# Kernel tuning notes

Measured on AMD Instinct MI355X. Metric: run time of the kernel, lower is better.

The kernel has to match this reference:

```python
import jax, jax.numpy as jnp
import numpy as np

EPS = 1e-8  # torch F.cosine_similarity eps


def setup_inputs() -> dict:
    key = jax.random.key(0)
    k1, k2 = jax.random.split(key)
    z = jax.random.normal(k1, (32768, 2048), dtype=jnp.float32)
    expert_keys = jax.random.normal(k2, (64, 2048), dtype=jnp.float32)
    return {"z": z, "expert_keys": expert_keys}


def reference(z, expert_keys):
    # cosine similarity: (z . ek) / max(||z||*||ek||, eps)  -> [N, E]
    dots = jnp.einsum("nd,ed->ne", z, expert_keys)
    z_norm = jnp.linalg.norm(z, axis=-1)            # [N]
    e_norm = jnp.linalg.norm(expert_keys, axis=-1)  # [E]
    similarity = dots / jnp.maximum(z_norm[:, None] * e_norm[None, :], EPS)
    # softmax over experts, then weighted combination of expert keys -> [N, D]
    weighted_expert = jax.nn.softmax(similarity, axis=-1) @ expert_keys
    return similarity, weighted_expert
```

## Files before the change

### kernel.cpp

```cpp
#include <hip/hip_runtime.h>
#include <hip/hip_bf16.h>

typedef __attribute__((ext_vector_type(4))) float f32x4;
typedef __attribute__((ext_vector_type(8))) short bf16x8;

#define NROWS 32768
#define DIM   2048
#define NEXP  64

__device__ __forceinline__ short f2bf(float f) {
    __hip_bfloat16 h = __float2bfloat16(f);
    short s;
    __builtin_memcpy(&s, &h, 2);
    return s;
}

__global__ __launch_bounds__(256) void prep_experts(
    const float* __restrict__ ek,
    short* __restrict__ ekbf,
    short* __restrict__ ekT,
    float* __restrict__ enorm)
{
    const int e = blockIdx.x;
    const int t = threadIdx.x;
    const float* row = ek + e * DIM;
    float ss = 0.f;
#pragma unroll
    for (int i = 0; i < 2; ++i) {
        const int c4 = t + i * 256;
        const float4 v = ((const float4*)row)[c4];
        ss += v.x * v.x + v.y * v.y + v.z * v.z + v.w * v.w;
        short4 b;
        b.x = f2bf(v.x); b.y = f2bf(v.y); b.z = f2bf(v.z); b.w = f2bf(v.w);
        *(short4*)(ekbf + e * DIM + c4 * 4) = b;
        const int d = c4 * 4;
        ekT[(d + 0) * NEXP + e] = b.x;
        ekT[(d + 1) * NEXP + e] = b.y;
        ekT[(d + 2) * NEXP + e] = b.z;
        ekT[(d + 3) * NEXP + e] = b.w;
    }
#pragma unroll
    for (int s = 1; s < 64; s <<= 1) ss += __shfl_xor(ss, s);
    __shared__ float red[4];
    if ((t & 63) == 0) red[t >> 6] = ss;
    __syncthreads();
    if (t == 0) enorm[e] = sqrtf(red[0] + red[1] + red[2] + red[3]);
}

__global__ __launch_bounds__(256) void cosmoe_main(
    const float* __restrict__ z,
    const short* __restrict__ ekbf,
    const short* __restrict__ ekT,
    const float* __restrict__ enorm,
    float* __restrict__ out_sim,
    float* __restrict__ out_wei)
{
    const int tid = threadIdx.x;
    const int w   = tid >> 6;
    const int l   = tid & 63;
    const int lr  = l & 15;
    const int lg  = l >> 4;
    const int base_row = blockIdx.x * 64;

    const float* zrow = z + (size_t)(base_row + w * 16 + lr) * DIM + lg * 8;
    f32x4 acc[4];
#pragma unroll
    for (int nt = 0; nt < 4; ++nt) acc[nt] = f32x4{0.f, 0.f, 0.f, 0.f};
    float ssq = 0.f;

    for (int kk = 0; kk < DIM / 32; ++kk) {
        const float4 a0 = *(const float4*)(zrow + kk * 32);
        const float4 a1 = *(const float4*)(zrow + kk * 32 + 4);
        ssq += a0.x * a0.x + a0.y * a0.y + a0.z * a0.z + a0.w * a0.w
             + a1.x * a1.x + a1.y * a1.y + a1.z * a1.z + a1.w * a1.w;
        bf16x8 af;
        af[0] = f2bf(a0.x); af[1] = f2bf(a0.y); af[2] = f2bf(a0.z); af[3] = f2bf(a0.w);
        af[4] = f2bf(a1.x); af[5] = f2bf(a1.y); af[6] = f2bf(a1.z); af[7] = f2bf(a1.w);
        const int koff = kk * 32 + lg * 8;
#pragma unroll
        for (int nt = 0; nt < 4; ++nt) {
            const bf16x8 bf = *(const bf16x8*)(ekbf + (nt * 16 + lr) * DIM + koff);
            acc[nt] = __builtin_amdgcn_mfma_f32_16x16x32_bf16(af, bf, acc[nt], 0, 0, 0);
        }
    }
    ssq += __shfl_xor(ssq, 16);
    ssq += __shfl_xor(ssq, 32);
    const float zn_mine = sqrtf(ssq);

    float zn_j[4];
#pragma unroll
    for (int j = 0; j < 4; ++j) zn_j[j] = __shfl(zn_mine, lg * 4 + j);
    float en_nt[4];
#pragma unroll
    for (int nt = 0; nt < 4; ++nt) en_nt[nt] = enorm[nt * 16 + lr];

    float sim[4][4];
#pragma unroll
    for (int j = 0; j < 4; ++j)
#pragma unroll
        for (int nt = 0; nt < 4; ++nt)
            sim[nt][j] = acc[nt][j] / fmaxf(zn_j[j] * en_nt[nt], 1e-8f);

#pragma unroll
    for (int j = 0; j < 4; ++j) {
        const size_t ro = (size_t)(base_row + w * 16 + lg * 4 + j) * NEXP + lr;
#pragma unroll
        for (int nt = 0; nt < 4; ++nt) out_sim[ro + nt * 16] = sim[nt][j];
    }

    float wgt[4][4];
#pragma unroll
    for (int j = 0; j < 4; ++j) {
        float mx = fmaxf(fmaxf(sim[0][j], sim[1][j]), fmaxf(sim[2][j], sim[3][j]));
#pragma unroll
        for (int s = 1; s < 16; s <<= 1) mx = fmaxf(mx, __shfl_xor(mx, s));
        float sum = 0.f;
#pragma unroll
        for (int nt = 0; nt < 4; ++nt) { wgt[nt][j] = __expf(sim[nt][j] - mx); sum += wgt[nt][j]; }
#pragma unroll
        for (int s = 1; s < 16; s <<= 1) sum += __shfl_xor(sum, s);
        const float inv = 1.0f / sum;
#pragma unroll
        for (int nt = 0; nt < 4; ++nt) wgt[nt][j] *= inv;
    }

    __shared__ __align__(16) short Wl[4][16][72];
#pragma unroll
    for (int j = 0; j < 4; ++j)
#pragma unroll
        for (int nt = 0; nt < 4; ++nt)
            Wl[w][lg * 4 + j][nt * 16 + lr] = f2bf(wgt[nt][j]);
    __syncthreads();

    bf16x8 afr[4][2];
#pragma unroll
    for (int mt = 0; mt < 4; ++mt)
#pragma unroll
        for (int ks = 0; ks < 2; ++ks)
            afr[mt][ks] = *(const bf16x8*)&Wl[mt][lr][ks * 32 + lg * 8];

    for (int ntl = 0; ntl < 32; ++ntl) {
        const int d0 = w * 512 + ntl * 16;
        const short* bp = ekT + (size_t)(d0 + lr) * NEXP + lg * 8;
        const bf16x8 b0 = *(const bf16x8*)bp;
        const bf16x8 b1 = *(const bf16x8*)(bp + 32);
        f32x4 oacc[4];
#pragma unroll
        for (int mt = 0; mt < 4; ++mt) {
            oacc[mt] = f32x4{0.f, 0.f, 0.f, 0.f};
            oacc[mt] = __builtin_amdgcn_mfma_f32_16x16x32_bf16(afr[mt][0], b0, oacc[mt], 0, 0, 0);
            oacc[mt] = __builtin_amdgcn_mfma_f32_16x16x32_bf16(afr[mt][1], b1, oacc[mt], 0, 0, 0);
        }
#pragma unroll
        for (int mt = 0; mt < 4; ++mt)
#pragma unroll
            for (int j = 0; j < 4; ++j)
                out_wei[(size_t)(base_row + mt * 16 + lg * 4 + j) * DIM + d0 + lr] = oacc[mt][j];
    }
}

extern "C" void kernel_launch(void* const* d_in, const int* in_sizes, int n_in,
                              void* d_out, int out_size, void* d_ws, size_t ws_size,
                              hipStream_t stream) {
    const float* z  = (const float*)d_in[0];
    const float* ek = (const float*)d_in[1];
    float* out_sim = (float*)d_out;
    float* out_wei = out_sim + (size_t)NROWS * NEXP;

    short* ekbf  = (short*)d_ws;
    short* ekT   = ekbf + NEXP * DIM;
    float* enorm = (float*)(ekT + DIM * NEXP);

    prep_experts<<<NEXP, 256, 0, stream>>>(ek, ekbf, ekT, enorm);
    cosmoe_main<<<NROWS / 64, 256, 0, stream>>>(z, ekbf, ekT, enorm, out_sim, out_wei);
}
```

Before: 162.2 us.

## Split fused kernel into split-K similarity and tiled softmax-combine kernels

Replaces the single fused kernel with two kernels. The first computes similarities with the K dimension split across the four waves of a block and reduced through shared memory, giving more blocks and shorter dependency chains. The second re-reads the similarity matrix, computes softmax, and multiplies by the expert keys over a 2D grid, staging outputs in LDS so each global store writes float4s across contiguous columns. In exchange the similarity output makes an extra round trip through global memory and there is one more launch.

Result: slower. 171.3 us (+5.6%).

```diff
diff --git a/kernel.cpp b/kernel.cpp
--- a/kernel.cpp
+++ b/kernel.cpp
@@ -47,12 +47,87 @@
     if (t == 0) enorm[e] = sqrtf(red[0] + red[1] + red[2] + red[3]);
 }
 
-__global__ __launch_bounds__(256) void cosmoe_main(
+__global__ __launch_bounds__(256) void sim_kernel(
     const float* __restrict__ z,
     const short* __restrict__ ekbf,
+    const float* __restrict__ enorm,
+    float* __restrict__ out_sim)
+{
+    const int tid = threadIdx.x;
+    const int w   = tid >> 6;
+    const int l   = tid & 63;
+    const int lr  = l & 15;
+    const int lg  = l >> 4;
+    const int base = blockIdx.x * 16;
+
+    __shared__ float racc[4][64][20];
+    __shared__ float rssq[4][16];
+
+    const float* zp = z    + (size_t)(base + lr) * DIM + w * 512 + lg * 8;
+    const short* ep = ekbf + (size_t)lr * DIM          + w * 512 + lg * 8;
+
+    f32x4 acc[4];
+#pragma unroll
+    for (int nt = 0; nt < 4; ++nt) acc[nt] = f32x4{0.f, 0.f, 0.f, 0.f};
+    float s0 = 0.f, s1 = 0.f;
+
+#pragma unroll 4
+    for (int c = 0; c < 16; ++c) {
+        const float4 a0 = *(const float4*)(zp + c * 32);
+        const float4 a1 = *(const float4*)(zp + c * 32 + 4);
+        s0 = fmaf(a0.x, a0.x, s0); s1 = fmaf(a0.y, a0.y, s1);
+        s0 = fmaf(a0.z, a0.z, s0); s1 = fmaf(a0.w, a0.w, s1);
+        s0 = fmaf(a1.x, a1.x, s0); s1 = fmaf(a1.y, a1.y, s1);
+        s0 = fmaf(a1.z, a1.z, s0); s1 = fmaf(a1.w, a1.w, s1);
+        bf16x8 af;
+        af[0] = f2bf(a0.x); af[1] = f2bf(a0.y); af[2] = f2bf(a0.z); af[3] = f2bf(a0.w);
+        af[4] = f2bf(a1.x); af[5] = f2bf(a1.y); af[6] = f2bf(a1.z); af[7] = f2bf(a1.w);
+#pragma unroll
+        for (int nt = 0; nt < 4; ++nt) {
+            const bf16x8 bf = *(const bf16x8*)(ep + nt * 16 * DIM + c * 32);
+            acc[nt] = __builtin_amdgcn_mfma_f32_16x16x32_bf16(af, bf, acc[nt], 0, 0, 0);
+        }
+    }
+    float ssq = s0 + s1;
+    ssq += __shfl_xor(ssq, 16);
+    ssq += __shfl_xor(ssq, 32);
+
+#pragma unroll
+    for (int nt = 0; nt < 4; ++nt)
+        *(f32x4*)&racc[w][l][nt * 4] = acc[nt];
+    if (l < 16) rssq[w][l] = ssq;
+    __syncthreads();
+
+    if (w == 0) {
+        f32x4 tot[4];
+#pragma unroll
+        for (int nt = 0; nt < 4; ++nt) {
+            tot[nt] = *(const f32x4*)&racc[0][l][nt * 4];
+#pragma unroll
+            for (int w2 = 1; w2 < 4; ++w2)
+                tot[nt] += *(const f32x4*)&racc[w2][l][nt * 4];
+        }
+        const float sq = rssq[0][lr] + rssq[1][lr] + rssq[2][lr] + rssq[3][lr];
+        const float zn = sqrtf(sq);
+        float zn_j[4];
+#pragma unroll
+        for (int j = 0; j < 4; ++j) zn_j[j] = __shfl(zn, lg * 4 + j);
+        float en_nt[4];
+#pragma unroll
+        for (int nt = 0; nt < 4; ++nt) en_nt[nt] = enorm[nt * 16 + lr];
+#pragma unroll
+        for (int j = 0; j < 4; ++j) {
+            const size_t ro = (size_t)(base + lg * 4 + j) * NEXP + lr;
+#pragma unroll
+            for (int nt = 0; nt < 4; ++nt)
+                out_sim[ro + nt * 16] = tot[nt][j] / fmaxf(zn_j[j] * en_nt[nt], 1e-8f);
+        }
+    }
+}
+
+__global__ __launch_bounds__(256) void moe_kernel(
+    const float* __restrict__ sim,
     const short* __restrict__ ekT,
-    const float* __restrict__ enorm,
-    float* __restrict__ out_sim,
     float* __restrict__ out_wei)
 {
     const int tid = threadIdx.x;
@@ -60,102 +135,80 @@
     const int l   = tid & 63;
     const int lr  = l & 15;
     const int lg  = l >> 4;
-    const int base_row = blockIdx.x * 64;
-
-    const float* zrow = z + (size_t)(base_row + w * 16 + lr) * DIM + lg * 8;
-    f32x4 acc[4];
-#pragma unroll
-    for (int nt = 0; nt < 4; ++nt) acc[nt] = f32x4{0.f, 0.f, 0.f, 0.f};
-    float ssq = 0.f;
-
-    for (int kk = 0; kk < DIM / 32; ++kk) {
-        const float4 a0 = *(const float4*)(zrow + kk * 32);
-        const float4 a1 = *(const float4*)(zrow + kk * 32 + 4);
-        ssq += a0.x * a0.x + a0.y * a0.y + a0.z * a0.z + a0.w * a0.w
-             + a1.x * a1.x + a1.y * a1.y + a1.z * a1.z + a1.w * a1.w;
-        bf16x8 af;
-        af[0] = f2bf(a0.x); af[1] = f2bf(a0.y); af[2] = f2bf(a0.z); af[3] = f2bf(a0.w);
-        af[4] = f2bf(a1.x); af[5] = f2bf(a1.y); af[6] = f2bf(a1.z); af[7] = f2bf(a1.w);
-        const int koff = kk * 32 + lg * 8;
-#pragma unroll
-        for (int nt = 0; nt < 4; ++nt) {
-            const bf16x8 bf = *(const bf16x8*)(ekbf + (nt * 16 + lr) * DIM + koff);
-            acc[nt] = __builtin_amdgcn_mfma_f32_16x16x32_bf16(af, bf, acc[nt], 0, 0, 0);
-        }
-    }
-    ssq += __shfl_xor(ssq, 16);
-    ssq += __shfl_xor(ssq, 32);
-    const float zn_mine = sqrtf(ssq);
-
-    float zn_j[4];
-#pragma unroll
-    for (int j = 0; j < 4; ++j) zn_j[j] = __shfl(zn_mine, lg * 4 + j);
-    float en_nt[4];
-#pragma unroll
-    for (int nt = 0; nt < 4; ++nt) en_nt[nt] = enorm[nt * 16 + lr];
-
-    float sim[4][4];
-#pragma unroll
-    for (int j = 0; j < 4; ++j)
-#pragma unroll
-        for (int nt = 0; nt < 4; ++nt)
-            sim[nt][j] = acc[nt][j] / fmaxf(zn_j[j] * en_nt[nt], 1e-8f);
-
-#pragma unroll
-    for (int j = 0; j < 4; ++j) {
-        const size_t ro = (size_t)(base_row + w * 16 + lg * 4 + j) * NEXP + lr;
-#pragma unroll
-        for (int nt = 0; nt < 4; ++nt) out_sim[ro + nt * 16] = sim[nt][j];
-    }
-
-    float wgt[4][4];
-#pragma unroll
-    for (int j = 0; j < 4; ++j) {
-        float mx = fmaxf(fmaxf(sim[0][j], sim[1][j]), fmaxf(sim[2][j], sim[3][j]));
-#pragma unroll
-        for (int s = 1; s < 16; s <<= 1) mx = fmaxf(mx, __shfl_xor(mx, s));
+    const int base = blockIdx.x * 32;
+    const int col0 = blockIdx.y * 1024 + w * 256;
+
+    __shared__ __align__(16) short WL[32][64];
+    __shared__ __align__(16) float tbuf[4][32][68];
+
+    {
+        const int r  = tid >> 3;
+        const int cc = tid & 7;
+        const float* sp = sim + (size_t)(base + r) * NEXP + cc * 8;
+        const float4 v0 = *(const float4*)sp;
+        const float4 v1 = *(const float4*)(sp + 4);
+        float va[8] = {v0.x, v0.y, v0.z, v0.w, v1.x, v1.y, v1.z, v1.w};
+        float m = va[0];
+#pragma unroll
+        for (int i = 1; i < 8; ++i) m = fmaxf(m, va[i]);
+        m = fmaxf(m, __shfl_xor(m, 1));
+        m = fmaxf(m, __shfl_xor(m, 2));
+        m = fmaxf(m, __shfl_xor(m, 4));
         float sum = 0.f;
 #pragma unroll
-        for (int nt = 0; nt < 4; ++nt) { wgt[nt][j] = __expf(sim[nt][j] - mx); sum += wgt[nt][j]; }
-#pragma unroll
-        for (int s = 1; s < 16; s <<= 1) sum += __shfl_xor(sum, s);
+        for (int i = 0; i < 8; ++i) { va[i] = __expf(va[i] - m); sum += va[i]; }
+        sum += __shfl_xor(sum, 1);
+        sum += __shfl_xor(sum, 2);
+        sum += __shfl_xor(sum, 4);
         const float inv = 1.0f / sum;
-#pragma unroll
-        for (int nt = 0; nt < 4; ++nt) wgt[nt][j] *= inv;
-    }
-
-    __shared__ __align__(16) short Wl[4][16][72];
-#pragma unroll
-    for (int j = 0; j < 4; ++j)
-#pragma unroll
-        for (int nt = 0; nt < 4; ++nt)
-            Wl[w][lg * 4 + j][nt * 16 + lr] = f2bf(wgt[nt][j]);
+        bf16x8 wv;
+#pragma unroll
+        for (int i = 0; i < 8; ++i) wv[i] = f2bf(va[i] * inv);
+        *(bf16x8*)&WL[r][(cc ^ (r & 7)) * 8] = wv;
+    }
     __syncthreads();
 
-    bf16x8 afr[4][2];
-#pragma unroll
-    for (int mt = 0; mt < 4; ++mt)
-#pragma unroll
-        for (int ks = 0; ks < 2; ++ks)
-            afr[mt][ks] = *(const bf16x8*)&Wl[mt][lr][ks * 32 + lg * 8];
-
-    for (int ntl = 0; ntl < 32; ++ntl) {
-        const int d0 = w * 512 + ntl * 16;
-        const short* bp = ekT + (size_t)(d0 + lr) * NEXP + lg * 8;
-        const bf16x8 b0 = *(const bf16x8*)bp;
-        const bf16x8 b1 = *(const bf16x8*)(bp + 32);
-        f32x4 oacc[4];
-#pragma unroll
-        for (int mt = 0; mt < 4; ++mt) {
-            oacc[mt] = f32x4{0.f, 0.f, 0.f, 0.f};
-            oacc[mt] = __builtin_amdgcn_mfma_f32_16x16x32_bf16(afr[mt][0], b0, oacc[mt], 0, 0, 0);
-            oacc[mt] = __builtin_amdgcn_mfma_f32_16x16x32_bf16(afr[mt][1], b1, oacc[mt], 0, 0, 0);
-        }
-#pragma unroll
-        for (int mt = 0; mt < 4; ++mt)
-#pragma unroll
-            for (int j = 0; j < 4; ++j)
-                out_wei[(size_t)(base_row + mt * 16 + lg * 4 + j) * DIM + d0 + lr] = oacc[mt][j];
+    bf16x8 afr[2][2];
+#pragma unroll
+    for (int mt = 0; mt < 2; ++mt)
+#pragma unroll
+        for (int ks = 0; ks < 2; ++ks) {
+            const int row = mt * 16 + lr;
+            const int u   = (ks * 4 + lg) ^ (row & 7);
+            afr[mt][ks] = *(const bf16x8*)&WL[row][u * 8];
+        }
+
+#pragma unroll 1
+    for (int g = 0; g < 4; ++g) {
+        f32x4 oacc[4][2];
+#pragma unroll
+        for (int nt2 = 0; nt2 < 4; ++nt2) {
+            const int d0 = col0 + g * 64 + nt2 * 16;
+            const short* bp = ekT + (size_t)(d0 + lr) * NEXP + lg * 8;
+            const bf16x8 b0 = *(const bf16x8*)bp;
+            const bf16x8 b1 = *(const bf16x8*)(bp + 32);
+#pragma unroll
+            for (int mt = 0; mt < 2; ++mt) {
+                f32x4 o = f32x4{0.f, 0.f, 0.f, 0.f};
+                o = __builtin_amdgcn_mfma_f32_16x16x32_bf16(afr[mt][0], b0, o, 0, 0, 0);
+                o = __builtin_amdgcn_mfma_f32_16x16x32_bf16(afr[mt][1], b1, o, 0, 0, 0);
+                oacc[nt2][mt] = o;
+            }
+        }
+#pragma unroll
+        for (int nt2 = 0; nt2 < 4; ++nt2)
+#pragma unroll
+            for (int mt = 0; mt < 2; ++mt)
+#pragma unroll
+                for (int j = 0; j < 4; ++j)
+                    tbuf[w][mt * 16 + lg * 4 + j][nt2 * 16 + lr] = oacc[nt2][mt][j];
+#pragma unroll
+        for (int i = 0; i < 8; ++i) {
+            const int row  = (l >> 4) + i * 4;
+            const int unit = l & 15;
+            const float4 t = *(const float4*)&tbuf[w][row][unit * 4];
+            *(float4*)&out_wei[(size_t)(base + row) * DIM + col0 + g * 64 + unit * 4] = t;
+        }
     }
 }
 
@@ -172,5 +225,6 @@
     float* enorm = (float*)(ekT + DIM * NEXP);
 
     prep_experts<<<NEXP, 256, 0, stream>>>(ek, ekbf, ekT, enorm);
-    cosmoe_main<<<NROWS / 64, 256, 0, stream>>>(z, ekbf, ekT, enorm, out_sim, out_wei);
-}
+    sim_kernel<<<NROWS / 16, 256, 0, stream>>>(z, ekbf, enorm, out_sim);
+    moe_kernel<<<dim3(NROWS / 32, 2), 256, 0, stream>>>(out_sim, ekT, out_wei);
+}
```
